# Kernel tuning notes

Measured on AMD Instinct MI355X. Metric: run time of the kernel, lower is better.

Reference implementation:

```python
import jax, jax.numpy as jnp
import numpy as np

B, IN_C, CH = 16384, 128, 512
EMBED_DIM = 6240          # = 64*64 + 64 + 64*32 + 32 (BatchDecoder param count)
NUM_EMB = 512
DEC_IN, DEC_H, DATA_Y = 64, 64, 32


def setup_inputs() -> dict:
    key = jax.random.key(0)
    ks = jax.random.split(key, 16)
    s = lambda fan_in: 1.0 / np.sqrt(fan_in)
    return {
        "x":   jax.random.normal(ks[0], (B, IN_C), jnp.float32),
        # enc_f: Linear(IN_C,CH) -> ReLU -> Linear(CH,EMBED_DIM)
        "Wf1": jax.random.normal(ks[1], (IN_C, CH), jnp.float32) * s(IN_C),
        "bf1": jax.random.normal(ks[2], (CH,), jnp.float32) * s(IN_C),
        "Wf2": jax.random.normal(ks[3], (CH, EMBED_DIM), jnp.float32) * s(CH),
        "bf2": jax.random.normal(ks[4], (EMBED_DIM,), jnp.float32) * s(CH),
        # enc_x: Linear(IN_C,CH) -> ReLU -> Linear(CH,DEC_IN)
        "Wx1": jax.random.normal(ks[5], (IN_C, CH), jnp.float32) * s(IN_C),
        "bx1": jax.random.normal(ks[6], (CH,), jnp.float32) * s(IN_C),
        "Wx2": jax.random.normal(ks[7], (CH, DEC_IN), jnp.float32) * s(CH),
        "bx2": jax.random.normal(ks[8], (DEC_IN,), jnp.float32) * s(CH),
        # VQ codebook: [dim, num_embeddings] as in Quantize
        "embed": jax.random.normal(ks[9], (EMBED_DIM, NUM_EMB), jnp.float32),
        # BatchDecoder per-codeword MLP parameters (nets' own init params;
        # the original's weight-injection loop is a no-op: `p = new_vec` only
        # rebinds a local, so the nets run with their initialized weights)
        "W1": jax.random.normal(ks[10], (NUM_EMB, DEC_IN, DEC_H), jnp.float32) * s(DEC_IN),
        "b1": jax.random.normal(ks[11], (NUM_EMB, DEC_H), jnp.float32) * s(DEC_IN),
        "W2": jax.random.normal(ks[12], (NUM_EMB, DEC_H, DATA_Y), jnp.float32) * s(DEC_H),
        "b2": jax.random.normal(ks[13], (NUM_EMB, DATA_Y), jnp.float32) * s(DEC_H),
    }


def reference(x, Wf1, bf1, Wf2, bf2, Wx1, bx1, Wx2, bx2, embed, W1, b1, W2, b2):
    # ---- encode: enc_f MLP -> [B, EMBED_DIM] ----
    pre_f = jax.nn.relu(x @ Wf1 + bf1) @ Wf2 + bf2
    # ---- Quantize (eval mode; EMA buffer updates are side effects only) ----
    # dist[b,k] = ||pre_f[b]||^2 - 2 pre_f[b].embed[:,k] + ||embed[:,k]||^2
    dist = (jnp.sum(pre_f * pre_f, axis=1, keepdims=True)
            - 2.0 * (pre_f @ embed)
            + jnp.sum(embed * embed, axis=0, keepdims=True))  # [B, K]
    embed_ind = jnp.argmin(dist, axis=1)                       # [B]
    encodings = jax.nn.one_hot(embed_ind, NUM_EMB, dtype=pre_f.dtype)
    quantize = embed.T[embed_ind]                              # [B, EMBED_DIM]
    diff = jnp.mean((jax.lax.stop_gradient(quantize) - pre_f) ** 2)
    z_q = pre_f + jax.lax.stop_gradient(quantize - pre_f)      # straight-through (unused by buggy decoder)
    avg_probs = jnp.mean(encodings, axis=0)
    perplexity = jnp.exp(-jnp.sum(avg_probs * jnp.log(avg_probs + 1e-10)))
    # ---- enc_x MLP -> [B, DEC_IN] ----
    embedded_x = jax.nn.relu(x @ Wx1 + bx1) @ Wx2 + bx2
    # ---- BatchDecoder: per-sample expert MLP dispatch by embed_ind ----
    h = jax.nn.relu(jnp.einsum('bi,bih->bh', embedded_x, W1[embed_ind]) + b1[embed_ind])
    dec = jnp.einsum('bh,bho->bo', h, W2[embed_ind]) + b2[embed_ind]  # [B, DATA_Y]
    return (dec, diff, embed_ind, perplexity)
```

## Files before the change

### kernel.cpp

```cpp
#include <hip/hip_runtime.h>
#include <math.h>

#define BN     16384
#define INC    128
#define CH     512
#define ED     6240
#define KN     512
#define DIN    64
#define DH     64
#define DY     32
#define NCW    195
#define CHP    (CH + 8)

#define OUT_DEC   0
#define OUT_DIFF  (BN*DY)
#define OUT_IND   (BN*DY + 1)
#define OUT_PERP  (BN*DY + 1 + BN)

typedef _Float16 half8 __attribute__((ext_vector_type(8)));
typedef float    f32x4 __attribute__((ext_vector_type(4)));
#define MFMA16(a, b, c) __builtin_amdgcn_mfma_f32_16x16x32_f16(a, b, c, 0, 0, 0)

__device__ __forceinline__ size_t paddr(int tile, int NC, int c, int lane, int e) {
    return ((size_t)(tile * NC + c) * 64 + lane) * 8 + e;
}

__global__ __launch_bounds__(256) void packall_kernel(
        const float* __restrict__ x,
        const float* __restrict__ Wf1, const float* __restrict__ Wx1,
        const float* __restrict__ bf1, const float* __restrict__ bx1,
        const float* __restrict__ Wx2,
        const float* __restrict__ Wf2, const float* __restrict__ bf2,
        const float* __restrict__ embed,
        _Float16* __restrict__ XPs, _Float16* __restrict__ XPl,
        _Float16* __restrict__ WfxPs, _Float16* __restrict__ WfxPl,
        float* __restrict__ bfx,
        _Float16* __restrict__ Wx2Ps, _Float16* __restrict__ Wx2Pl,
        _Float16* __restrict__ WfPs, _Float16* __restrict__ WfPl,
        _Float16* __restrict__ EmPs, _Float16* __restrict__ EmPl,
        float* __restrict__ s2p, float* __restrict__ bep,
        float* __restrict__ w0) {
    __shared__ __align__(16) char smem[16384];
    int id = blockIdx.x;
    int t = threadIdx.x;
    if (id < 12480) {
        float (*red)[33] = (float(*)[33])smem;
        int bx = id % NCW, by = id / NCW;
        int d = bx * 32 + (t & 31);
        int j = by * 8 + (t >> 5);
        float v = Wf2[(size_t)j * ED + d];
        _Float16 hi = (_Float16)v;
        size_t a = paddr(j >> 4, NCW, d >> 5, ((d & 31) >> 3) * 16 + (j & 15), d & 7);
        WfPs[a] = hi;
        WfPl[a] = (_Float16)(v - (float)hi);
        red[t >> 5][t & 31] = v * bf2[d];
        __syncthreads();
        if (t < 8) {
            float s = 0.f;
            #pragma unroll
            for (int i = 0; i < 32; ++i) s += red[t][i];
            atomicAdd(&w0[by * 8 + t], s);
        }
    } else if (id < 15600) {
        float (*tile)[33] = (float(*)[33])smem;
        int sub = id - 12480;
        int bx = sub % NCW, by = sub / NCW;
        int dl = t >> 5, kl = t & 31;
        #pragma unroll
        for (int r = 0; r < 4; ++r)
            tile[dl + 8 * r][kl] = embed[(size_t)(bx * 32 + dl + 8 * r) * KN
                                         + by * 32 + kl];
        __syncthreads();
        int d = bx * 32 + kl;
        #pragma unroll
        for (int r = 0; r < 4; ++r) {
            int k = by * 32 + dl + 8 * r;
            float v = tile[kl][dl + 8 * r];
            _Float16 hi = (_Float16)v;
            size_t a = paddr(k >> 4, NCW, d >> 5, ((d & 31) >> 3) * 16 + (k & 15), d & 7);
            EmPs[a] = hi;
            EmPl[a] = (_Float16)(v - (float)hi);
        }
    } else if (id < 15728) {
        float (*rs)[33] = (float(*)[33])smem;
        float (*rb)[33] = (float(*)[33])(smem + 8 * 33 * 4);
        int sub = id - 15600;
        int bx = sub % 16, by = sub / 16;
        int kl = t & 31, dl = t >> 5;
        int kb = bx * 32;
        int d0 = by * 780;
        float s = 0.f, b = 0.f;
        for (int d = d0 + dl; d < d0 + 780; d += 8) {
            float e = embed[(size_t)d * KN + kb + kl];
            s = fmaf(e, e, s);
            b = fmaf(bf2[d], e, b);
        }
        rs[dl][kl] = s; rb[dl][kl] = b;
        __syncthreads();
        if (t < 32) {
            float ss = 0.f, bb = 0.f;
            #pragma unroll
            for (int i = 0; i < 8; ++i) { ss += rs[i][t]; bb += rb[i][t]; }
            s2p[by * KN + kb + t] = ss;
            bep[by * KN + kb + t] = bb;
        }
    } else if (id < 16240) {
        float (*xt)[INC] = (float(*)[INC])smem;
        int m0 = (id - 15728) * 32;
        for (int i = t; i < 32 * (INC / 4); i += 256) {
            int row = i >> 5, c4 = (i & 31) << 2;
            *(float4*)&xt[row][c4] = *(const float4*)&x[(size_t)(m0 + row) * INC + c4];
        }
        __syncthreads();
        int ta = m0 >> 4;
        #pragma unroll
        for (int i = 0; i < 2; ++i) {
            int idx = t + 256 * i;
            int tile2 = idx >> 8;
            int c = (idx >> 6) & 3;
            int lane = idx & 63;
            int m = tile2 * 16 + (lane & 15);
            int d0 = c * 32 + ((lane >> 4) << 3);
            half8 hh, ll;
            #pragma unroll
            for (int e = 0; e < 8; ++e) {
                float v = xt[m][d0 + e];
                _Float16 hi = (_Float16)v;
                hh[e] = hi;
                ll[e] = (_Float16)(v - (float)hi);
            }
            *(half8*)(XPs + paddr(ta + tile2, 4, c, lane, 0)) = hh;
            *(half8*)(XPl + paddr(ta + tile2, 4, c, lane, 0)) = ll;
        }
    } else if (id < 16304) {
        int tile = id - 16240;
        for (int i = t; i < 2048; i += 256) {
            int c = i >> 9, lane = (i >> 3) & 63, e = i & 7;
            int n = tile * 16 + (lane & 15);
            int d = c * 32 + ((lane >> 4) << 3) + e;
            float v = (n < 512) ? Wf1[(size_t)d * CH + n] : Wx1[(size_t)d * CH + n - 512];
            _Float16 hi = (_Float16)v;
            size_t a = paddr(tile, 4, c, lane, e);
            WfxPs[a] = hi;
            WfxPl[a] = (_Float16)(v - (float)hi);
        }
        if (tile == 0)
            for (int j = t; j < 512; j += 256) { bfx[j] = bf1[j]; bfx[512 + j] = bx1[j]; }
    } else {
        int tile = id - 16304;
        for (int i = t; i < 8192; i += 256) {
            int c = i >> 9, lane = (i >> 3) & 63, e = i & 7;
            int n = tile * 16 + (lane & 15);
            int d = c * 32 + ((lane >> 4) << 3) + e;
            float v = Wx2[(size_t)d * DIN + n];
            _Float16 hi = (_Float16)v;
            size_t a = paddr(tile, 16, c, lane, e);
            Wx2Ps[a] = hi;
            Wx2Pl[a] = (_Float16)(v - (float)hi);
        }
    }
}

__global__ __launch_bounds__(512) void mfma_weg_kernel(
        const _Float16* __restrict__ WfPs, const _Float16* __restrict__ WfPl,
        const _Float16* __restrict__ EmPs, const _Float16* __restrict__ EmPl,
        float* __restrict__ WeP, float* __restrict__ GP) {
    int t = threadIdx.x;
    int w = t >> 6, L = t & 63;
    int lane16 = L & 15, quad = L >> 4;
    int m0 = blockIdx.x * 128 + (w & 3) * 32;
    int n0 = blockIdx.y * 128 + (w >> 2) * 64;
    int ta = m0 >> 4, tb = n0 >> 4;
    int zraw = blockIdx.z;
    bool isWe = zraw < 8;
    int z = isWe ? zraw : zraw - 8;
    int base = NCW / 8, rem = NCW % 8;
    int c0 = z * base + (z < rem ? z : rem);
    int cnt = base + (z < rem ? 1 : 0);
    f32x4 acc[2][4];
    #pragma unroll
    for (int rt = 0; rt < 2; ++rt)
        #pragma unroll
        for (int tt = 0; tt < 4; ++tt) acc[rt][tt] = (f32x4){0.f, 0.f, 0.f, 0.f};
    if (isWe) {
        for (int ci = 0; ci < cnt; ++ci) {
            int c = c0 + ci;
            size_t oa0 = paddr(ta, NCW, c, L, 0), oa1 = paddr(ta + 1, NCW, c, L, 0);
            half8 A0h = *(const half8*)(WfPs + oa0);
            half8 A0l = *(const half8*)(WfPl + oa0);
            half8 A1h = *(const half8*)(WfPs + oa1);
            half8 A1l = *(const half8*)(WfPl + oa1);
            #pragma unroll
            for (int tt = 0; tt < 4; ++tt) {
                size_t ob = paddr(tb + tt, NCW, c, L, 0);
                half8 Bh = *(const half8*)(EmPs + ob);
                half8 Bl8 = *(const half8*)(EmPl + ob);
                acc[0][tt] = MFMA16(A0h, Bl8, MFMA16(A0l, Bh, MFMA16(A0h, Bh, acc[0][tt])));
                acc[1][tt] = MFMA16(A1h, Bl8, MFMA16(A1l, Bh, MFMA16(A1h, Bh, acc[1][tt])));
            }
        }
    } else {
        for (int ci = 0; ci < cnt; ++ci) {
            int c = c0 + ci;
            half8 A0h = *(const half8*)(WfPs + paddr(ta, NCW, c, L, 0));
            half8 A1h = *(const half8*)(WfPs + paddr(ta + 1, NCW, c, L, 0));
            #pragma unroll
            for (int tt = 0; tt < 4; ++tt) {
                half8 Bh = *(const half8*)(WfPs + paddr(tb + tt, NCW, c, L, 0));
                acc[0][tt] = MFMA16(A0h, Bh, acc[0][tt]);
                acc[1][tt] = MFMA16(A1h, Bh, acc[1][tt]);
            }
        }
    }
    float* C = (isWe ? WeP : GP) + (size_t)z * KN * KN;
    #pragma unroll
    for (int rt = 0; rt < 2; ++rt)
        #pragma unroll
        for (int tt = 0; tt < 4; ++tt)
            #pragma unroll
            for (int r = 0; r < 4; ++r)
                C[(size_t)(m0 + rt * 16 + quad * 4 + r) * KN
                  + n0 + tt * 16 + lane16] = acc[rt][tt][r];
}

__global__ __launch_bounds__(256) void wepackgred_kernel(
        const float* __restrict__ WeP, const float* __restrict__ GP,
        const float* __restrict__ s2p, const float* __restrict__ bep,
        _Float16* __restrict__ WePs, _Float16* __restrict__ WePl,
        _Float16* __restrict__ GhPs, float* __restrict__ s2,
        float* __restrict__ be) {
    int id = blockIdx.x;
    int t = threadIdx.x;
    if (id < 1024) {
        int g = id * 256 + t;
        int j = g >> 9, k = g & 511;
        float v = 0.f;
        #pragma unroll
        for (int z = 0; z < 8; ++z) v += WeP[(size_t)z * KN * KN + g];
        _Float16 hi = (_Float16)v;
        size_t a = paddr(k >> 4, 16, j >> 5, ((j & 31) >> 3) * 16 + (k & 15), j & 7);
        WePs[a] = hi;
        WePl[a] = (_Float16)(v - (float)hi);
    } else if (id < 2048) {
        int g = (id - 1024) * 256 + t;
        int m = g >> 9, n = g & 511;
        float v = 0.f;
        #pragma unroll
        for (int z = 0; z < 8; ++z) v += GP[(size_t)z * KN * KN + g];
        GhPs[paddr(n >> 4, 16, m >> 5, ((m & 31) >> 3) * 16 + (n & 15), m & 7)]
            = (_Float16)v;
    } else {
        #pragma unroll
        for (int i = 0; i < 2; ++i) {
            int k = t + 256 * i;
            float s = 0.f, b = 0.f;
            #pragma unroll
            for (int y = 0; y < 8; ++y) {
                s += s2p[y * KN + k];
                b += bep[y * KN + k];
            }
            s2[k] = s;
            be[k] = b;
        }
    }
}

__global__ __launch_bounds__(512) void enc1_kernel(
        const _Float16* __restrict__ XPs, const _Float16* __restrict__ XPl,
        const _Float16* __restrict__ WfxPs, const _Float16* __restrict__ WfxPl,
        const float* __restrict__ bfx,
        const _Float16* __restrict__ Wx2Ps, const _Float16* __restrict__ Wx2Pl,
        const float* __restrict__ bx2,
        const _Float16* __restrict__ WePs, const _Float16* __restrict__ WePl,
        const _Float16* __restrict__ GhPs,
        const float* __restrict__ s2, const float* __restrict__ be,
        float* __restrict__ colsum,
        float* __restrict__ EX,
        int* __restrict__ ind, float* __restrict__ out_ind,
        int* __restrict__ counts, float* __restrict__ diffsum) {
    __shared__ _Float16 hhi[32][CHP];
    __shared__ _Float16 hlo[32][CHP];
    __shared__ float redv[8][32];
    __shared__ int   redi[8][32];
    __shared__ float fin[32];
    __shared__ float gpart[8];
    int t = threadIdx.x;
    int w = t >> 6, L = t & 63;
    int l16 = L & 15, quad = L >> 4;
    int enc = blockIdx.x;
    int m0 = blockIdx.y * 32;
    int ta = m0 >> 4;
    int n0 = enc * 512 + w * 64;
    int tb = n0 >> 4;
    f32x4 acc[2][4];
    #pragma unroll
    for (int rt = 0; rt < 2; ++rt)
        #pragma unroll
        for (int tt = 0; tt < 4; ++tt) acc[rt][tt] = (f32x4){0.f, 0.f, 0.f, 0.f};
    #pragma unroll
    for (int c = 0; c < 4; ++c) {
        size_t oa0 = paddr(ta, 4, c, L, 0), oa1 = paddr(ta + 1, 4, c, L, 0);
        half8 A0h = *(const half8*)(XPs + oa0);
        half8 A0l = *(const half8*)(XPl + oa0);
        half8 A1h = *(const half8*)(XPs + oa1);
        half8 A1l = *(const half8*)(XPl + oa1);
        #pragma unroll
        for (int tt = 0; tt < 4; ++tt) {
            size_t ob = paddr(tb + tt, 4, c, L, 0);
            half8 Bh = *(const half8*)(WfxPs + ob);
            half8 Bl8 = *(const half8*)(WfxPl + ob);
            acc[0][tt] = MFMA16(A0h, Bl8, MFMA16(A0l, Bh, MFMA16(A0h, Bh, acc[0][tt])));
            acc[1][tt] = MFMA16(A1h, Bl8, MFMA16(A1l, Bh, MFMA16(A1h, Bh, acc[1][tt])));
        }
    }
    float colp[4] = {0.f, 0.f, 0.f, 0.f};
    #pragma unroll
    for (int rt = 0; rt < 2; ++rt)
        #pragma unroll
        for (int tt = 0; tt < 4; ++tt) {
            int col = w * 64 + tt * 16 + l16;
            float bias = bfx[enc * 512 + col];
            #pragma unroll
            for (int r = 0; r < 4; ++r) {
                int row = rt * 16 + quad * 4 + r;
                float v = fmaxf(acc[rt][tt][r] + bias, 0.f);
                _Float16 hi = (_Float16)v;
                hhi[row][col] = hi;
                hlo[row][col] = (_Float16)(v - (float)hi);
                colp[tt] += v;
            }
        }
    __syncthreads();
    if (enc == 0) {
        #pragma unroll
        for (int tt = 0; tt < 4; ++tt) {
            float s = colp[tt];
            s += __shfl_xor(s, 16);
            s += __shfl_xor(s, 32);
            if (quad == 0) atomicAdd(&colsum[w * 64 + tt * 16 + l16], s);
        }
        int colbase = w * 64;
        int tbs = w * 4;
        float cks[4];
        #pragma unroll
        for (int tt = 0; tt < 4; ++tt) {
            int c = colbase + tt * 16 + l16;
            cks[tt] = 0.5f * s2[c] - be[c];
        }
        #pragma unroll
        for (int rt = 0; rt < 2; ++rt)
            #pragma unroll
            for (int tt = 0; tt < 4; ++tt) acc[rt][tt] = (f32x4){0.f, 0.f, 0.f, 0.f};
        const _Float16* hA0 = &hhi[l16][quad << 3];
        const _Float16* lA0 = &hlo[l16][quad << 3];
        const _Float16* hA1 = &hhi[16 + l16][quad << 3];
        const _Float16* lA1 = &hlo[16 + l16][quad << 3];
        #pragma unroll 2
        for (int c = 0; c < 16; ++c) {
            int d0 = c * 32;
            half8 A0h = *(const half8*)(hA0 + d0);
            half8 A0l = *(const half8*)(lA0 + d0);
            half8 A1h = *(const half8*)(hA1 + d0);
            half8 A1l = *(const half8*)(lA1 + d0);
            #pragma unroll
            for (int tt = 0; tt < 4; ++tt) {
                size_t ob = paddr(tbs + tt, 16, c, L, 0);
                half8 Bh = *(const half8*)(WePs + ob);
                half8 Bl8 = *(const half8*)(WePl + ob);
                acc[0][tt] = MFMA16(A0h, Bl8, MFMA16(A0l, Bh, MFMA16(A0h, Bh, acc[0][tt])));
                acc[1][tt] = MFMA16(A1h, Bl8, MFMA16(A1l, Bh, MFMA16(A1h, Bh, acc[1][tt])));
            }
        }
        #pragma unroll
        for (int rt = 0; rt < 2; ++rt) {
            #pragma unroll
            for (int r = 0; r < 4; ++r) {
                float mv = cks[0] - acc[rt][0][r];
                int mi = colbase + l16;
                #pragma unroll
                for (int tt = 1; tt < 4; ++tt) {
                    float v = cks[tt] - acc[rt][tt][r];
                    int c = colbase + tt * 16 + l16;
                    if (v < mv || (v == mv && c < mi)) { mv = v; mi = c; }
                }
                #pragma unroll
                for (int d = 1; d < 16; d <<= 1) {
                    float ov = __shfl_xor(mv, d);
                    int oi = __shfl_xor(mi, d);
                    if (ov < mv || (ov == mv && oi < mi)) { mv = ov; mi = oi; }
                }
                if (l16 == 0) {
                    int row = rt * 16 + quad * 4 + r;
                    redv[w][row] = mv; redi[w][row] = mi;
                }
            }
        }
        #pragma unroll
        for (int rt = 0; rt < 2; ++rt)
            #pragma unroll
            for (int tt = 0; tt < 4; ++tt) acc[rt][tt] = (f32x4){0.f, 0.f, 0.f, 0.f};
        #pragma unroll 2
        for (int c = 0; c < 16; ++c) {
            int d0 = c * 32;
            half8 A0h = *(const half8*)(hA0 + d0);
            half8 A1h = *(const half8*)(hA1 + d0);
            #pragma unroll
            for (int tt = 0; tt < 4; ++tt) {
                half8 Gh = *(const half8*)(GhPs + paddr(tbs + tt, 16, c, L, 0));
                acc[0][tt] = MFMA16(A0h, Gh, acc[0][tt]);
                acc[1][tt] = MFMA16(A1h, Gh, acc[1][tt]);
            }
        }
        float gs = 0.f;
        #pragma unroll
        for (int rt = 0; rt < 2; ++rt)
            #pragma unroll
            for (int tt = 0; tt < 4; ++tt) {
                int col = colbase + tt * 16 + l16;
                #pragma unroll
                for (int r = 0; r < 4; ++r) {
                    int row = rt * 16 + quad * 4 + r;
                    gs += acc[rt][tt][r] * (float)hhi[row][col];
                }
            }
        #pragma unroll
        for (int d = 1; d < 64; d <<= 1) gs += __shfl_xor(gs, d);
        if (L == 0) gpart[w] = gs;
        __syncthreads();
        if (t < 32) {
            float mv = redv[0][t]; int mi = redi[0][t];
            #pragma unroll
            for (int w2 = 1; w2 < 8; ++w2) {
                float ov = redv[w2][t]; int oi = redi[w2][t];
                if (ov < mv || (ov == mv && oi < mi)) { mv = ov; mi = oi; }
            }
            int b = m0 + t;
            ind[b] = mi;
            out_ind[b] = (float)mi;
            atomicAdd(&counts[mi], 1);
            fin[t] = 2.f * mv;
        }
        __syncthreads();
        if (t == 0) {
            float s = 0.f;
            #pragma unroll
            for (int i = 0; i < 32; ++i) s += fin[i];
            #pragma unroll
            for (int w2 = 0; w2 < 8; ++w2) s += gpart[w2];
            atomicAdd(diffsum, s);
        }
    } else {
        int rt = w & 1, ct = w >> 1;
        f32x4 eacc = (f32x4){0.f, 0.f, 0.f, 0.f};
        for (int c = 0; c < 16; ++c) {
            int d0 = c * 32 + (quad << 3);
            int m = rt * 16 + l16;
            half8 Ah = *(half8*)(&hhi[m][d0]);
            half8 Al = *(half8*)(&hlo[m][d0]);
            size_t ob = paddr(ct, 16, c, L, 0);
            half8 Bh = *(const half8*)(Wx2Ps + ob);
            half8 Bl8 = *(const half8*)(Wx2Pl + ob);
            eacc = MFMA16(Ah, Bl8, MFMA16(Al, Bh, MFMA16(Ah, Bh, eacc)));
        }
        int col = ct * 16 + l16;
        float bias = bx2[col];
        #pragma unroll
        for (int r = 0; r < 4; ++r) {
            int row = m0 + rt * 16 + quad * 4 + r;
            EX[(size_t)row * DIN + col] = eacc[r] + bias;
        }
    }
}

__global__ __launch_bounds__(512) void finalize_kernel(const int* __restrict__ counts,
                                                       const float* __restrict__ diffsum,
                                                       const float* __restrict__ colsum,
                                                       const float* __restrict__ w0,
                                                       const float* __restrict__ bf2,
                                                       float* __restrict__ out_diff,
                                                       float* __restrict__ out_perp) {
    __shared__ float sf[512];
    int t = threadIdx.x;
    int c = counts[t];
    double p = (double)c / (double)BN;
    double term = -p * log(p + 1e-10);
    float dotp = colsum[t] * w0[t];
    float bbp = 0.f;
    for (int d = t; d < ED; d += 512) { float v = bf2[d]; bbp = fmaf(v, v, bbp); }
    sf[t] = dotp; __syncthreads();
    for (int s = 256; s > 0; s >>= 1) { if (t < s) sf[t] += sf[t + s]; __syncthreads(); }
    float dot_all = sf[0];
    __syncthreads();
    sf[t] = bbp; __syncthreads();
    for (int s = 256; s > 0; s >>= 1) { if (t < s) sf[t] += sf[t + s]; __syncthreads(); }
    float bb = sf[0];
    __syncthreads();
    sf[t] = (float)term; __syncthreads();
    for (int s = 256; s > 0; s >>= 1) { if (t < s) sf[t] += sf[t + s]; __syncthreads(); }
    if (t == 0) {
        *out_perp = expf(sf[0]);
        *out_diff = (diffsum[0] + 2.f * dot_all + (float)BN * bb) /
                    ((float)BN * (float)ED);
    }
}

__global__ __launch_bounds__(256) void scatter_kernel(const int* __restrict__ ind,
                                                      const int* __restrict__ counts,
                                                      int* __restrict__ cursors,
                                                      int* __restrict__ perm) {
    __shared__ int sc[KN], soff[KN], lcount[KN], lbase[KN], lcur[KN];
    int t = threadIdx.x;
    for (int i = t; i < KN; i += 256) {
        sc[i] = counts[i];
        lcount[i] = 0; lcur[i] = 0;
    }
    __syncthreads();
    #pragma unroll
    for (int half = 0; half < 2; ++half) {
        int i = t + 256 * half;
        int off = 0;
        for (int k = 0; k < i; ++k) off += sc[k];
        soff[i] = off;
    }
    int b = blockIdx.x * 256 + t;
    int k = ind[b];
    atomicAdd(&lcount[k], 1);
    __syncthreads();
    for (int i = t; i < KN; i += 256) {
        int c = lcount[i];
        if (c > 0) lbase[i] = atomicAdd(&cursors[i], c);
    }
    __syncthreads();
    int pos = soff[k] + lbase[k] + atomicAdd(&lcur[k], 1);
    perm[pos] = b;
}

__global__ __launch_bounds__(256) void decode_kernel(const float* __restrict__ EX,
                                                     const int* __restrict__ perm,
                                                     const int* __restrict__ ind,
                                                     const float* __restrict__ W1,
                                                     const float* __restrict__ b1,
                                                     const float* __restrict__ W2,
                                                     const float* __restrict__ b2,
                                                     float* __restrict__ dec) {
    __shared__ float exs[4][DIN];
    __shared__ float h2s[4][DH];
    int t = threadIdx.x;
    int w = t >> 6, l = t & 63;
    int s = blockIdx.x * 4 + w;
    int b = perm[s];
    int k = ind[b];
    exs[w][l] = EX[(size_t)b * DIN + l];
    __syncthreads();
    const float* w1 = W1 + (size_t)k * (DIN * DH);
    float h = b1[(size_t)k * DH + l];
    #pragma unroll
    for (int j = 0; j < DIN; ++j)
        h = fmaf(exs[w][j], w1[(size_t)j * DH + l], h);
    h2s[w][l] = fmaxf(h, 0.f);
    __syncthreads();
    if (l < DY) {
        const float* w2 = W2 + (size_t)k * (DH * DY);
        float d = b2[(size_t)k * DY + l];
        #pragma unroll
        for (int j = 0; j < DH; ++j)
            d = fmaf(h2s[w][j], w2[(size_t)j * DY + l], d);
        dec[(size_t)b * DY + l] = d;
    }
}

extern "C" void kernel_launch(void* const* d_in, const int* in_sizes, int n_in,
                              void* d_out, int out_size, void* d_ws, size_t ws_size,
                              hipStream_t stream) {
    const float* x     = (const float*)d_in[0];
    const float* Wf1   = (const float*)d_in[1];
    const float* bf1   = (const float*)d_in[2];
    const float* Wf2   = (const float*)d_in[3];
    const float* bf2   = (const float*)d_in[4];
    const float* Wx1   = (const float*)d_in[5];
    const float* bx1   = (const float*)d_in[6];
    const float* Wx2   = (const float*)d_in[7];
    const float* bx2   = (const float*)d_in[8];
    const float* embed = (const float*)d_in[9];
    const float* W1    = (const float*)d_in[10];
    const float* b1    = (const float*)d_in[11];
    const float* W2    = (const float*)d_in[12];
    const float* b2    = (const float*)d_in[13];
    float* out = (float*)d_out;

    char* ws = (char*)d_ws;
    size_t off = 0;
    auto carve = [&](size_t bytes) -> void* {
        void* p = ws + off;
        off += (bytes + 255) & ~(size_t)255;
        return p;
    };
    _Float16* XPs   = (_Float16*)carve((size_t)BN * INC * 2);
    _Float16* XPl   = (_Float16*)carve((size_t)BN * INC * 2);
    _Float16* WfxPs = (_Float16*)carve((size_t)1024 * INC * 2);
    _Float16* WfxPl = (_Float16*)carve((size_t)1024 * INC * 2);
    float*    bfx   = (float*)carve(1024 * 4);
    _Float16* Wx2Ps = (_Float16*)carve((size_t)DIN * CH * 2);
    _Float16* Wx2Pl = (_Float16*)carve((size_t)DIN * CH * 2);
    _Float16* WfPs  = (_Float16*)carve((size_t)CH * ED * 2);
    _Float16* WfPl  = (_Float16*)carve((size_t)CH * ED * 2);
    _Float16* EmPs  = (_Float16*)carve((size_t)KN * ED * 2);
    _Float16* EmPl  = (_Float16*)carve((size_t)KN * ED * 2);
    char* un = (char*)carve((size_t)BN * CH * 2);
    float*    WeP = (float*)un;
    float*    GP  = (float*)(un + (size_t)8 * KN * KN * 4);
    _Float16* WePs = (_Float16*)carve((size_t)KN * CH * 2);
    _Float16* WePl = (_Float16*)carve((size_t)KN * CH * 2);
    _Float16* GhPs = (_Float16*)carve((size_t)KN * KN * 2);
    float*    EX   = (float*)carve((size_t)BN * DIN * 4);
    float*    s2p  = (float*)carve(8 * KN * 4);
    float*    bep  = (float*)carve(8 * KN * 4);
    float*    s2   = (float*)carve(KN * 4);
    float*    be   = (float*)carve(KN * 4);
    char* zbase = ws + off;
    float* w0    = (float*)carve(CH * 4);
    float* colsum= (float*)carve(CH * 4);
    int*   counts= (int*)carve(KN * 4);
    int*   cursors=(int*)carve(KN * 4);
    float* diffsum=(float*)carve(256);
    size_t zbytes = (size_t)(ws + off - zbase);
    int*   ind     = (int*)carve(BN * 4);
    int*   perm    = (int*)carve(BN * 4);
    (void)in_sizes; (void)n_in; (void)out_size; (void)ws_size;

    hipMemsetAsync(zbase, 0, zbytes, stream);
    packall_kernel<<<16308, 256, 0, stream>>>(x, Wf1, Wx1, bf1, bx1, Wx2, Wf2, bf2,
                                              embed, XPs, XPl, WfxPs, WfxPl, bfx,
                                              Wx2Ps, Wx2Pl, WfPs, WfPl, EmPs, EmPl,
                                              s2p, bep, w0);
    mfma_weg_kernel<<<dim3(4, 4, 16), 512, 0, stream>>>(WfPs, WfPl, EmPs, EmPl,
                                                        WeP, GP);
    wepackgred_kernel<<<2049, 256, 0, stream>>>(WeP, GP, s2p, bep,
                                                WePs, WePl, GhPs, s2, be);
    enc1_kernel<<<dim3(2, BN / 32), 512, 0, stream>>>(XPs, XPl, WfxPs, WfxPl, bfx,
                                                      Wx2Ps, Wx2Pl, bx2,
                                                      WePs, WePl, GhPs, s2, be,
                                                      colsum, EX,
                                                      ind, out + OUT_IND, counts,
                                                      diffsum);
    scatter_kernel<<<BN / 256, 256, 0, stream>>>(ind, counts, cursors, perm);
    decode_kernel<<<BN / 4, 256, 0, stream>>>(EX, perm, ind, W1, b1, W2, b2,
                                              out + OUT_DEC);
    finalize_kernel<<<1, 512, 0, stream>>>(counts, diffsum, colsum, w0, bf2,
                                           out + OUT_DIFF, out + OUT_PERP);
}
```

Measured before the change: 365.0 us.

## Fold finalize into decode launch, swap enc1 grid axes, simplify colsum

Removes the separate single-block finalize launch by appending an extra block to the decode kernel that computes perplexity and diff. Swaps the enc1 grid dimensions so that the two encoder halves of one row tile are no longer adjacent block indices. Computes the colsum from the shared-memory hi/lo halves instead of from per-lane partials with shuffles. Drops the unroll-2 pragmas on the distance loops. The fused finalize block depends on scatter/enc1 having completed, which still holds because it runs in a later kernel, and the reconstructed colsum adds a small fp16-split rounding difference.

```diff
diff --git a/kernel.cpp b/kernel.cpp
--- a/kernel.cpp
+++ b/kernel.cpp
@@ -287,9 +287,9 @@
     int t = threadIdx.x;
     int w = t >> 6, L = t & 63;
     int l16 = L & 15, quad = L >> 4;
-    int enc = blockIdx.x;
-    int m0 = blockIdx.y * 32;
+    int m0 = blockIdx.x * 32;
     int ta = m0 >> 4;
+    int enc = blockIdx.y;
     int n0 = enc * 512 + w * 64;
     int tb = n0 >> 4;
     f32x4 acc[2][4];
@@ -313,7 +313,6 @@
             acc[1][tt] = MFMA16(A1h, Bl8, MFMA16(A1l, Bh, MFMA16(A1h, Bh, acc[1][tt])));
         }
     }
-    float colp[4] = {0.f, 0.f, 0.f, 0.f};
     #pragma unroll
     for (int rt = 0; rt < 2; ++rt)
         #pragma unroll
@@ -327,18 +326,14 @@
                 _Float16 hi = (_Float16)v;
                 hhi[row][col] = hi;
                 hlo[row][col] = (_Float16)(v - (float)hi);
-                colp[tt] += v;
             }
         }
     __syncthreads();
     if (enc == 0) {
-        #pragma unroll
-        for (int tt = 0; tt < 4; ++tt) {
-            float s = colp[tt];
-            s += __shfl_xor(s, 16);
-            s += __shfl_xor(s, 32);
-            if (quad == 0) atomicAdd(&colsum[w * 64 + tt * 16 + l16], s);
-        }
+        float s = 0.f;
+        #pragma unroll
+        for (int r = 0; r < 32; ++r) s += (float)hhi[r][t] + (float)hlo[r][t];
+        atomicAdd(&colsum[t], s);
         int colbase = w * 64;
         int tbs = w * 4;
         float cks[4];
@@ -355,7 +350,6 @@
         const _Float16* lA0 = &hlo[l16][quad << 3];
         const _Float16* hA1 = &hhi[16 + l16][quad << 3];
         const _Float16* lA1 = &hlo[16 + l16][quad << 3];
-        #pragma unroll 2
         for (int c = 0; c < 16; ++c) {
             int d0 = c * 32;
             half8 A0h = *(const half8*)(hA0 + d0);
@@ -399,7 +393,6 @@
         for (int rt = 0; rt < 2; ++rt)
             #pragma unroll
             for (int tt = 0; tt < 4; ++tt) acc[rt][tt] = (f32x4){0.f, 0.f, 0.f, 0.f};
-        #pragma unroll 2
         for (int c = 0; c < 16; ++c) {
             int d0 = c * 32;
             half8 A0h = *(const half8*)(hA0 + d0);
@@ -472,38 +465,6 @@
     }
 }
 
-__global__ __launch_bounds__(512) void finalize_kernel(const int* __restrict__ counts,
-                                                       const float* __restrict__ diffsum,
-                                                       const float* __restrict__ colsum,
-                                                       const float* __restrict__ w0,
-                                                       const float* __restrict__ bf2,
-                                                       float* __restrict__ out_diff,
-                                                       float* __restrict__ out_perp) {
-    __shared__ float sf[512];
-    int t = threadIdx.x;
-    int c = counts[t];
-    double p = (double)c / (double)BN;
-    double term = -p * log(p + 1e-10);
-    float dotp = colsum[t] * w0[t];
-    float bbp = 0.f;
-    for (int d = t; d < ED; d += 512) { float v = bf2[d]; bbp = fmaf(v, v, bbp); }
-    sf[t] = dotp; __syncthreads();
-    for (int s = 256; s > 0; s >>= 1) { if (t < s) sf[t] += sf[t + s]; __syncthreads(); }
-    float dot_all = sf[0];
-    __syncthreads();
-    sf[t] = bbp; __syncthreads();
-    for (int s = 256; s > 0; s >>= 1) { if (t < s) sf[t] += sf[t + s]; __syncthreads(); }
-    float bb = sf[0];
-    __syncthreads();
-    sf[t] = (float)term; __syncthreads();
-    for (int s = 256; s > 0; s >>= 1) { if (t < s) sf[t] += sf[t + s]; __syncthreads(); }
-    if (t == 0) {
-        *out_perp = expf(sf[0]);
-        *out_diff = (diffsum[0] + 2.f * dot_all + (float)BN * bb) /
-                    ((float)BN * (float)ED);
-    }
-}
-
 __global__ __launch_bounds__(256) void scatter_kernel(const int* __restrict__ ind,
                                                       const int* __restrict__ counts,
                                                       int* __restrict__ cursors,
@@ -542,30 +503,67 @@
                                                      const float* __restrict__ b1,
                                                      const float* __restrict__ W2,
                                                      const float* __restrict__ b2,
-                                                     float* __restrict__ dec) {
-    __shared__ float exs[4][DIN];
-    __shared__ float h2s[4][DH];
+                                                     float* __restrict__ dec,
+                                                     const int* __restrict__ counts,
+                                                     const float* __restrict__ diffsum,
+                                                     const float* __restrict__ colsum,
+                                                     const float* __restrict__ w0,
+                                                     const float* __restrict__ bf2,
+                                                     float* __restrict__ out_diff,
+                                                     float* __restrict__ out_perp) {
+    if (blockIdx.x < BN / 4) {
+        __shared__ float exs[4][DIN];
+        __shared__ float h2s[4][DH];
+        int t = threadIdx.x;
+        int w = t >> 6, l = t & 63;
+        int s = blockIdx.x * 4 + w;
+        int b = perm[s];
+        int k = ind[b];
+        exs[w][l] = EX[(size_t)b * DIN + l];
+        __syncthreads();
+        const float* w1 = W1 + (size_t)k * (DIN * DH);
+        float h = b1[(size_t)k * DH + l];
+        #pragma unroll
+        for (int j = 0; j < DIN; ++j)
+            h = fmaf(exs[w][j], w1[(size_t)j * DH + l], h);
+        h2s[w][l] = fmaxf(h, 0.f);
+        __syncthreads();
+        if (l < DY) {
+            const float* w2 = W2 + (size_t)k * (DH * DY);
+            float d = b2[(size_t)k * DY + l];
+            #pragma unroll
+            for (int j = 0; j < DH; ++j)
+                d = fmaf(h2s[w][j], w2[(size_t)j * DY + l], d);
+            dec[(size_t)b * DY + l] = d;
+        }
+        return;
+    }
+    __shared__ float sf[256];
     int t = threadIdx.x;
-    int w = t >> 6, l = t & 63;
-    int s = blockIdx.x * 4 + w;
-    int b = perm[s];
-    int k = ind[b];
-    exs[w][l] = EX[(size_t)b * DIN + l];
+    float term = 0.f, dotp = 0.f, bbp = 0.f;
+    #pragma unroll
+    for (int i = 0; i < 2; ++i) {
+        int k = t + 256 * i;
+        int c = counts[k];
+        double p = (double)c / (double)BN;
+        term += (float)(-p * log(p + 1e-10));
+        dotp += colsum[k] * w0[k];
+    }
+    for (int d = t; d < ED; d += 256) { float v = bf2[d]; bbp = fmaf(v, v, bbp); }
+    sf[t] = dotp; __syncthreads();
+    for (int s = 128; s > 0; s >>= 1) { if (t < s) sf[t] += sf[t + s]; __syncthreads(); }
+    float dot_all = sf[0];
     __syncthreads();
-    const float* w1 = W1 + (size_t)k * (DIN * DH);
-    float h = b1[(size_t)k * DH + l];
-    #pragma unroll
-    for (int j = 0; j < DIN; ++j)
-        h = fmaf(exs[w][j], w1[(size_t)j * DH + l], h);
-    h2s[w][l] = fmaxf(h, 0.f);
+    sf[t] = bbp; __syncthreads();
+    for (int s = 128; s > 0; s >>= 1) { if (t < s) sf[t] += sf[t + s]; __syncthreads(); }
+    float bb = sf[0];
     __syncthreads();
-    if (l < DY) {
-        const float* w2 = W2 + (size_t)k * (DH * DY);
-        float d = b2[(size_t)k * DY + l];
-        #pragma unroll
-        for (int j = 0; j < DH; ++j)
-            d = fmaf(h2s[w][j], w2[(size_t)j * DY + l], d);
-        dec[(size_t)b * DY + l] = d;
+    sf[t] = term; __syncthreads();
+    for (int s = 128; s > 0; s >>= 1) { if (t < s) sf[t] += sf[t + s]; __syncthreads(); }
+    if (t == 0) {
+        *out_perp = expf(sf[0]);
+        *out_diff = (diffsum[0] + 2.f * dot_all + (float)BN * bb) /
+                    ((float)BN * (float)ED);
     }
 }
 
@@ -637,15 +635,15 @@
                                                         WeP, GP);
     wepackgred_kernel<<<2049, 256, 0, stream>>>(WeP, GP, s2p, bep,
                                                 WePs, WePl, GhPs, s2, be);
-    enc1_kernel<<<dim3(2, BN / 32), 512, 0, stream>>>(XPs, XPl, WfxPs, WfxPl, bfx,
+    enc1_kernel<<<dim3(BN / 32, 2), 512, 0, stream>>>(XPs, XPl, WfxPs, WfxPl, bfx,
                                                       Wx2Ps, Wx2Pl, bx2,
                                                       WePs, WePl, GhPs, s2, be,
                                                       colsum, EX,
                                                       ind, out + OUT_IND, counts,
                                                       diffsum);
     scatter_kernel<<<BN / 256, 256, 0, stream>>>(ind, counts, cursors, perm);
-    decode_kernel<<<BN / 4, 256, 0, stream>>>(EX, perm, ind, W1, b1, W2, b2,
-                                              out + OUT_DEC);
-    finalize_kernel<<<1, 512, 0, stream>>>(counts, diffsum, colsum, w0, bf2,
-                                           out + OUT_DIFF, out + OUT_PERP);
-}
+    decode_kernel<<<BN / 4 + 1, 256, 0, stream>>>(EX, perm, ind, W1, b1, W2, b2,
+                                                  out + OUT_DEC,
+                                                  counts, diffsum, colsum, w0, bf2,
+                                                  out + OUT_DIFF, out + OUT_PERP);
+}
```

New measurement: 338.2 us. -7.4%, faster.
